# Kernel optimization log

Measured on AMD Instinct MI355X. Metric: run time of the kernel, lower is better.

The kernel has to match this reference:

```python
import jax, jax.numpy as jnp
import numpy as np

jax.config.update("jax_enable_x64", True)  # window_sum runs cumsums in double, as in the torch source

WIN = 7
EPS = 0.01


def _gradient(I):
    # forward finite differences, cropping to [D-1, H-1, W-1] (same=False path, reduction='mean')
    c = I[:, :, 1:, 1:, 1:]
    dx = c - I[:, :, :-1, 1:, 1:]
    dy = c - I[:, :, 1:, :-1, 1:]
    dz = c - I[:, :, 1:, 1:, :-1]
    return dx, dy, dz


def _window_sum(I, win):
    # 3D box-filter via triple cumsum on a zero-padded double-precision volume
    if win == 1:
        return I
    half = win // 2
    pad = (half + win % 2, half)
    Ip = jnp.pad(I, ((0, 0), (0, 0), pad, pad, pad)).astype(jnp.float64)
    cs = jnp.cumsum(jnp.cumsum(jnp.cumsum(Ip, axis=2), axis=3), axis=4)
    x, y, z = I.shape[2:]
    w = win
    out = (cs[:, :, w:, w:, w:] - cs[:, :, w:, w:, :z] - cs[:, :, w:, :y, w:]
           - cs[:, :, :x, w:, w:] + cs[:, :, w:, :y, :z] + cs[:, :, :x, w:, :z]
           + cs[:, :, :x, :y, w:] - cs[:, :, :x, :y, :z])
    return out.astype(jnp.float32)


def setup_inputs() -> dict:
    key = jax.random.key(0)
    k1, k2 = jax.random.split(key)
    shape = (2, 1, 160, 192, 160)
    Ii = jax.random.normal(k1, shape, dtype=jnp.float32)
    Ji = jax.random.normal(k2, shape, dtype=jnp.float32)
    return {"Ii": Ii, "Ji": Ji}


def reference(Ii, Ji):
    def det(dx, dy, dz):
        return dx * dx + dy * dy + dz * dz + EPS

    dxI, dyI, dzI = _gradient(Ii)
    dxJ, dyJ, dzJ = _gradient(Ji)
    dx_I = _window_sum(dxI, WIN)
    dy_I = _window_sum(dyI, WIN)
    dz_I = _window_sum(dzI, WIN)
    dx_J = _window_sum(dxJ, WIN)
    dy_J = _window_sum(dyJ, WIN)
    dz_J = _window_sum(dzJ, WIN)
    cross = jnp.abs(dx_I * dx_J + dy_I * dy_J + dz_I * dz_J) + EPS
    norm = jnp.sqrt(det(dx_I, dy_I, dz_I) * det(dx_J, dy_J, dz_J))
    return jnp.mean(cross / norm)
```

## Files before the change

kernel.cpp:

```cpp
#include <hip/hip_runtime.h>

#define IYD 192
#define IZD 160
#define PLANE 30720
#define VOLSZ 4915200
#define YG 191
#define ZG 159

#define RAWV 660
#define RAWR 44
#define ZBB 1324
#define DBB 2404
#define ZDV 540
#define ZDR 36
#define TBB 3484
#define WBB 3996
#define LDSF 4508

#define NVOX_INV (1.0f / 9657342.0f)

__global__ __launch_bounds__(256, 4) void grad_sim_v7(
    const float* __restrict__ Ii, const float* __restrict__ Ji,
    float* __restrict__ out)
{
    __shared__ __align__(16) float lds[LDSF];
    const int tid = threadIdx.x;
    const int z0 = (int)blockIdx.x * 32;
    const int y0 = (int)blockIdx.y * 8;
    const int seg = blockIdx.z & 3;
    const int bat = blockIdx.z >> 2;
    const int s0 = seg * 40;
    const int a0 = (seg == 0) ? 0 : (s0 - 3);
    const int aLast = (seg == 3) ? 159 : (s0 + 43);

    const float* __restrict__ bI = Ii + (size_t)bat * VOLSZ;
    const float* __restrict__ bJ = Ji + (size_t)bat * VOLSZ;

    const float* gq0;
    const float* gq1;
    int lq0, lq1;
    float mq0, mq1;
    {
        int q = tid;
        int v = q / 150;
        int rr = q - v * 150;
        int row = rr / 10;
        int qd = rr - row * 10;
        int iy = y0 - 3 + row;
        int izb = z0 - 4 + 4 * qd;
        bool ok = ((unsigned)iy < IYD) && (izb >= 0) && (izb + 3 <= 159);
        int iyc = min(max(iy, 0), IYD - 1);
        int izc = min(max(izb, 0), 156);
        gq0 = (v ? bJ : bI) + (iyc * IZD + izc);
        lq0 = v * RAWV + row * RAWR + 4 * qd;
        mq0 = ok ? 1.f : 0.f;
    }
    {
        int q = 256 + tid;
        int v = q / 150;
        int rr = q - v * 150;
        int row = rr / 10;
        int qd = rr - row * 10;
        int iy = y0 - 3 + row;
        int izb = z0 - 4 + 4 * qd;
        bool ok = ((unsigned)iy < IYD) && (izb >= 0) && (izb + 3 <= 159);
        int iyc = min(max(iy, 0), IYD - 1);
        int izc = min(max(izb, 0), 156);
        gq1 = (v ? bJ : bI) + (iyc * IZD + izc);
        lq1 = v * RAWV + row * RAWR + 4 * qd;
        mq1 = ok ? 1.f : 0.f;
    }

    const int zv = tid / 60;
    const int zrr = tid - 60 * zv;
    const int zr = zrr >> 2;
    const int zq = zrr & 3;
    const bool doZ = tid < 120;
    const bool zlo = (z0 == 0) && (zq == 0);
    const bool zhi = (z0 == 128) && (zq == 3);
    const int rawRd = zv * RAWV + zr * RAWR + 8 * zq;
    const int zdWr = zv * ZDV + zr * ZDR + 8 * zq;

    const int e2half = tid & 1;
    const int e2c = tid >> 1;
    const int e2zq = e2c & 7;
    const int e2f = (e2c >> 3) & 1;
    const int e2v = e2c >> 4;
    const bool doY = tid < 64;
    const int e2base = (e2f ? DBB : ZBB) + e2v * ZDV + 4 * e2zq;
    const int e2out = (e2f ? WBB : TBB) + e2v * 256 + 4 * e2zq;
    const float mlo = (y0 == 0) ? 0.f : 1.f;
    const float mhi = (y0 == 184) ? 0.f : 1.f;

    const int oy = tid >> 5;
    const int oz = tid & 31;
    const int ygl = y0 + oy;
    const int vmax = min(3, 190 - ygl);
    const int vmin = max(-3, -ygl);
    const int vHiI = ZBB + (oy + vmax + 4) * ZDR + oz;
    const int vLoI = ZBB + (oy + vmin + 3) * ZDR + oz;
    const bool okyz = (ygl < YG) && ((z0 + oz) < ZG);

    float Tr[2][8], Vr[2][8], Wr[2][8], Sdy[2], Sdz[2];
#pragma unroll
    for (int v = 0; v < 2; ++v) {
#pragma unroll
        for (int j = 0; j < 8; ++j) { Tr[v][j] = 0.f; Vr[v][j] = 0.f; Wr[v][j] = 0.f; }
        Sdy[v] = 0.f; Sdz[v] = 0.f;
    }
    float acc = 0.f;

    {
        const size_t pb = (size_t)a0 * PLANE;
        float4 t0 = *(const float4*)(gq0 + pb);
        t0.x *= mq0; t0.y *= mq0; t0.z *= mq0; t0.w *= mq0;
        *(float4*)&lds[lq0] = t0;
        if (tid < 44) {
            float4 t1 = *(const float4*)(gq1 + pb);
            t1.x *= mq1; t1.y *= mq1; t1.z *= mq1; t1.w *= mq1;
            *(float4*)&lds[lq1] = t1;
        }
    }
    __syncthreads();

    for (int ag = (a0 & ~7); ag <= aLast; ag += 8) {
#pragma unroll
        for (int u = 0; u < 8; ++u) {
            const int a = ag + u;
            if (a < a0 || a > aLast) continue;

            const bool dof = (a + 1) <= aLast;
            float4 pf0, pf1;
            if (dof) {
                const size_t pb = (size_t)(a + 1) * PLANE;
                pf0 = *(const float4*)(gq0 + pb);
                if (tid < 44) pf1 = *(const float4*)(gq1 + pb);
            }

            if (doZ) {
                float C[16];
                const float4* rb = (const float4*)&lds[rawRd];
#pragma unroll
                for (int q = 0; q < 4; ++q) ((float4*)C)[q] = rb[q];
                float D[8];
#pragma unroll
                for (int i = 0; i < 8; ++i) D[i] = C[i + 8] - C[i + 1];
                if (zlo) { D[0] = C[8] - C[4]; D[1] = C[9] - C[4]; D[2] = C[10] - C[4]; }
                if (zhi) { D[4] = C[11] - C[5]; D[5] = C[11] - C[6];
                           D[6] = C[11] - C[7]; D[7] = C[11] - C[8]; }
                if (zlo) { C[2] = 0.f; C[3] = 0.f; C[4] = 0.f; }
                float Z[8];
                float w = C[2] + C[3] + C[4] + C[5] + C[6] + C[7] + C[8];
                Z[0] = w;
#pragma unroll
                for (int m = 1; m < 8; ++m) { w += C[m + 8] - C[m + 1]; Z[m] = w; }
                float4* zb = (float4*)&lds[ZBB + zdWr];
                zb[0] = make_float4(Z[0], Z[1], Z[2], Z[3]);
                zb[1] = make_float4(Z[4], Z[5], Z[6], Z[7]);
                float4* db = (float4*)&lds[DBB + zdWr];
                db[0] = make_float4(D[0], D[1], D[2], D[3]);
                db[1] = make_float4(D[4], D[5], D[6], D[7]);
            }
            __syncthreads();

            if (doY) {
                float4 r[11];
                const int r0 = e2half ? 4 : 1;
#pragma unroll
                for (int i = 0; i < 11; ++i)
                    r[i] = *(const float4*)&lds[e2base + (r0 + i) * ZDR];
                if (e2half == 0) {
                    r[0].x *= mlo; r[0].y *= mlo; r[0].z *= mlo; r[0].w *= mlo;
                    r[1].x *= mlo; r[1].y *= mlo; r[1].z *= mlo; r[1].w *= mlo;
                    r[2].x *= mlo; r[2].y *= mlo; r[2].z *= mlo; r[2].w *= mlo;
                    r[10].x *= mhi; r[10].y *= mhi; r[10].z *= mhi; r[10].w *= mhi;
                    float4 w;
                    w.x = r[0].x + r[1].x + r[2].x + r[3].x + r[4].x + r[5].x + r[6].x;
                    w.y = r[0].y + r[1].y + r[2].y + r[3].y + r[4].y + r[5].y + r[6].y;
                    w.z = r[0].z + r[1].z + r[2].z + r[3].z + r[4].z + r[5].z + r[6].z;
                    w.w = r[0].w + r[1].w + r[2].w + r[3].w + r[4].w + r[5].w + r[6].w;
                    *(float4*)&lds[e2out] = w;
#pragma unroll
                    for (int m = 1; m < 4; ++m) {
                        w.x += r[m + 6].x - r[m - 1].x;
                        w.y += r[m + 6].y - r[m - 1].y;
                        w.z += r[m + 6].z - r[m - 1].z;
                        w.w += r[m + 6].w - r[m - 1].w;
                        *(float4*)&lds[e2out + m * 32] = w;
                    }
                } else {
                    r[7].x *= mhi; r[7].y *= mhi; r[7].z *= mhi; r[7].w *= mhi;
                    r[8].x *= mhi; r[8].y *= mhi; r[8].z *= mhi; r[8].w *= mhi;
                    r[9].x *= mhi; r[9].y *= mhi; r[9].z *= mhi; r[9].w *= mhi;
                    r[10].x *= mhi; r[10].y *= mhi; r[10].z *= mhi; r[10].w *= mhi;
                    float4 w;
                    w.x = r[1].x + r[2].x + r[3].x + r[4].x + r[5].x + r[6].x + r[7].x;
                    w.y = r[1].y + r[2].y + r[3].y + r[4].y + r[5].y + r[6].y + r[7].y;
                    w.z = r[1].z + r[2].z + r[3].z + r[4].z + r[5].z + r[6].z + r[7].z;
                    w.w = r[1].w + r[2].w + r[3].w + r[4].w + r[5].w + r[6].w + r[7].w;
                    *(float4*)&lds[e2out + 4 * 32] = w;
#pragma unroll
                    for (int m = 1; m < 4; ++m) {
                        w.x += r[m + 7].x - r[m].x;
                        w.y += r[m + 7].y - r[m].y;
                        w.z += r[m + 7].z - r[m].z;
                        w.w += r[m + 7].w - r[m].w;
                        *(float4*)&lds[e2out + (4 + m) * 32] = w;
                    }
                }
            }
            __syncthreads();

            {
                float tI = lds[TBB + tid];
                float tJ = lds[TBB + 256 + tid];
                float wI = lds[WBB + tid];
                float wJ = lds[WBB + 256 + tid];
                float vI = lds[vHiI] - lds[vLoI];
                float vJ = lds[vHiI + ZDV] - lds[vLoI + ZDV];
                if (a == a0) { vI = 0.f; vJ = 0.f; wI = 0.f; wJ = 0.f; }
                const int p = u;
                const int p1 = (u + 1) & 7;
                float hdxI = tI - Tr[0][p1];
                float hdxJ = tJ - Tr[1][p1];
                Sdy[0] += vI - Vr[0][p1]; Vr[0][p] = vI;
                Sdy[1] += vJ - Vr[1][p1]; Vr[1][p] = vJ;
                Sdz[0] += wI - Wr[0][p1]; Wr[0][p] = wI;
                Sdz[1] += wJ - Wr[1][p1]; Wr[1][p] = wJ;
                Tr[0][p] = tI; Tr[1][p] = tJ;
                if (p == 0 && a == 0) {
                    Tr[0][5] = tI; Tr[0][6] = tI; Tr[0][7] = tI;
                    Tr[1][5] = tJ; Tr[1][6] = tJ; Tr[1][7] = tJ;
                }
                if (a >= s0 + 4) {
                    float cross = fabsf(hdxI * hdxJ + Sdy[0] * Sdy[1] + Sdz[0] * Sdz[1]) + 0.01f;
                    float dI = hdxI * hdxI + Sdy[0] * Sdy[0] + Sdz[0] * Sdz[0] + 0.01f;
                    float dJ = hdxJ * hdxJ + Sdy[1] * Sdy[1] + Sdz[1] * Sdz[1] + 0.01f;
                    float val = cross * rsqrtf(dI * dJ);
                    if (okyz) acc += val;
                }
            }

            if (dof) {
                pf0.x *= mq0; pf0.y *= mq0; pf0.z *= mq0; pf0.w *= mq0;
                *(float4*)&lds[lq0] = pf0;
                if (tid < 44) {
                    pf1.x *= mq1; pf1.y *= mq1; pf1.z *= mq1; pf1.w *= mq1;
                    *(float4*)&lds[lq1] = pf1;
                }
            }
            __syncthreads();
        }
    }

    if (seg == 3) {
#pragma unroll
        for (int tt = 0; tt < 3; ++tt) {
            const int sl = tt + 1;
            float hdxI = Tr[0][7] - Tr[0][sl];
            float hdxJ = Tr[1][7] - Tr[1][sl];
            Sdy[0] -= Vr[0][sl]; Sdy[1] -= Vr[1][sl];
            Sdz[0] -= Wr[0][sl]; Sdz[1] -= Wr[1][sl];
            float cross = fabsf(hdxI * hdxJ + Sdy[0] * Sdy[1] + Sdz[0] * Sdz[1]) + 0.01f;
            float dI = hdxI * hdxI + Sdy[0] * Sdy[0] + Sdz[0] * Sdz[0] + 0.01f;
            float dJ = hdxJ * hdxJ + Sdy[1] * Sdy[1] + Sdz[1] * Sdz[1] + 0.01f;
            float val = cross * rsqrtf(dI * dJ);
            if (okyz) acc += val;
        }
    }

#pragma unroll
    for (int off = 32; off > 0; off >>= 1) acc += __shfl_down(acc, off, 64);
    __syncthreads();
    if ((tid & 63) == 0) lds[tid >> 6] = acc;
    __syncthreads();
    if (tid == 0)
        atomicAdd(out, (lds[0] + lds[1] + lds[2] + lds[3]) * NVOX_INV);
}

extern "C" void kernel_launch(void* const* d_in, const int* in_sizes, int n_in,
                              void* d_out, int out_size, void* d_ws, size_t ws_size,
                              hipStream_t stream) {
    const float* Ii = (const float*)d_in[0];
    const float* Ji = (const float*)d_in[1];
    float* out = (float*)d_out;
    hipMemsetAsync(d_out, 0, sizeof(float) * (out_size > 0 ? out_size : 1), stream);
    dim3 grid(5, 24, 8);
    grad_sim_v7<<<grid, dim3(256), 0, stream>>>(Ii, Ji, out);
}
```

Baseline: 77.73 us.

## Process two x-planes per barrier phase with double-buffered LDS stages

The plane loop now handles two consecutive x-planes per iteration. It uses double-buffered raw, Z/D and T/W LDS regions, so the z-pass and y-pass for both planes run in parallel across the two halves of the block. This roughly halves the number of __syncthreads per plane and prefetches two planes ahead to deepen the memory pipeline. In exchange, LDS use per block roughly doubles (about 36 KB), which may limit occupancy, and register pressure rises from the extra prefetch registers.

```diff
diff --git a/kernel.cpp b/kernel.cpp
--- a/kernel.cpp
+++ b/kernel.cpp
@@ -9,17 +9,26 @@
 
 #define RAWV 660
 #define RAWR 44
-#define ZBB 1324
-#define DBB 2404
+#define RAWSLOT 1320
+#define ZBA 2668
+#define DBA 3748
+#define ZBB2 4844
+#define DBB2 5924
+#define TBA 7004
+#define WBA 7516
+#define TBB2 8028
+#define WBB2 8540
 #define ZDV 540
 #define ZDR 36
-#define TBB 3484
-#define WBB 3996
-#define LDSF 4508
+#define LDSF 9052
 
 #define NVOX_INV (1.0f / 9657342.0f)
 
-__global__ __launch_bounds__(256, 4) void grad_sim_v7(
+__device__ __forceinline__ float4 f4scale(float4 a, float s) {
+    return make_float4(a.x * s, a.y * s, a.z * s, a.w * s);
+}
+
+__global__ __launch_bounds__(256, 4) void grad_sim_v12(
     const float* __restrict__ Ii, const float* __restrict__ Ji,
     float* __restrict__ out)
 {
@@ -36,59 +45,55 @@
     const float* __restrict__ bI = Ii + (size_t)bat * VOLSZ;
     const float* __restrict__ bJ = Ji + (size_t)bat * VOLSZ;
 
-    const float* gq0;
-    const float* gq1;
-    int lq0, lq1;
-    float mq0, mq1;
+    const float* gq0; const float* gq1;
+    int lq0, lq1; float mq0, mq1;
     {
         int q = tid;
-        int v = q / 150;
-        int rr = q - v * 150;
-        int row = rr / 10;
-        int qd = rr - row * 10;
-        int iy = y0 - 3 + row;
-        int izb = z0 - 4 + 4 * qd;
+        int v = q / 150; int rr = q - v * 150;
+        int row = rr / 10; int qd = rr - row * 10;
+        int iy = y0 - 3 + row; int izb = z0 - 4 + 4 * qd;
         bool ok = ((unsigned)iy < IYD) && (izb >= 0) && (izb + 3 <= 159);
-        int iyc = min(max(iy, 0), IYD - 1);
-        int izc = min(max(izb, 0), 156);
+        int iyc = min(max(iy, 0), IYD - 1); int izc = min(max(izb, 0), 156);
         gq0 = (v ? bJ : bI) + (iyc * IZD + izc);
         lq0 = v * RAWV + row * RAWR + 4 * qd;
         mq0 = ok ? 1.f : 0.f;
     }
     {
         int q = 256 + tid;
-        int v = q / 150;
-        int rr = q - v * 150;
-        int row = rr / 10;
-        int qd = rr - row * 10;
-        int iy = y0 - 3 + row;
-        int izb = z0 - 4 + 4 * qd;
+        int v = q / 150; int rr = q - v * 150;
+        int row = rr / 10; int qd = rr - row * 10;
+        int iy = y0 - 3 + row; int izb = z0 - 4 + 4 * qd;
         bool ok = ((unsigned)iy < IYD) && (izb >= 0) && (izb + 3 <= 159);
-        int iyc = min(max(iy, 0), IYD - 1);
-        int izc = min(max(izb, 0), 156);
+        int iyc = min(max(iy, 0), IYD - 1); int izc = min(max(izb, 0), 156);
         gq1 = (v ? bJ : bI) + (iyc * IZD + izc);
         lq1 = v * RAWV + row * RAWR + 4 * qd;
         mq1 = ok ? 1.f : 0.f;
     }
 
-    const int zv = tid / 60;
-    const int zrr = tid - 60 * zv;
-    const int zr = zrr >> 2;
-    const int zq = zrr & 3;
-    const bool doZ = tid < 120;
+    const int pp = tid >> 7;
+    const int rem = tid & 127;
+    const bool doZ = rem < 120;
+    const int e1t = doZ ? rem : 0;
+    const int zv = (e1t >= 60) ? 1 : 0;
+    const int rr1 = e1t - 60 * zv;
+    const int zr = rr1 >> 2;
+    const int zq = rr1 & 3;
     const bool zlo = (z0 == 0) && (zq == 0);
     const bool zhi = (z0 == 128) && (zq == 3);
-    const int rawRd = zv * RAWV + zr * RAWR + 8 * zq;
-    const int zdWr = zv * ZDV + zr * ZDR + 8 * zq;
-
-    const int e2half = tid & 1;
-    const int e2c = tid >> 1;
+    const int rawRd = pp * RAWSLOT + zv * RAWV + zr * RAWR + 8 * zq;
+    const int zbW = (pp ? ZBB2 : ZBA) + zv * ZDV + zr * ZDR + 8 * zq;
+    const int dbW = (pp ? DBB2 : DBA) + zv * ZDV + zr * ZDR + 8 * zq;
+
+    const int pp2 = (tid >> 6) & 1;
+    const bool doY = tid < 128;
+    const int et = tid & 63;
+    const int e2half = et & 1;
+    const int e2c = et >> 1;
     const int e2zq = e2c & 7;
     const int e2f = (e2c >> 3) & 1;
     const int e2v = e2c >> 4;
-    const bool doY = tid < 64;
-    const int e2base = (e2f ? DBB : ZBB) + e2v * ZDV + 4 * e2zq;
-    const int e2out = (e2f ? WBB : TBB) + e2v * 256 + 4 * e2zq;
+    const int e2base = (e2f ? (pp2 ? DBB2 : DBA) : (pp2 ? ZBB2 : ZBA)) + e2v * ZDV + 4 * e2zq;
+    const int e2out = (e2f ? (pp2 ? WBB2 : WBA) : (pp2 ? TBB2 : TBA)) + e2v * 256 + 4 * e2zq;
     const float mlo = (y0 == 0) ? 0.f : 1.f;
     const float mhi = (y0 == 184) ? 0.f : 1.f;
 
@@ -97,8 +102,8 @@
     const int ygl = y0 + oy;
     const int vmax = min(3, 190 - ygl);
     const int vmin = max(-3, -ygl);
-    const int vHiI = ZBB + (oy + vmax + 4) * ZDR + oz;
-    const int vLoI = ZBB + (oy + vmin + 3) * ZDR + oz;
+    const int vHiRel = (oy + vmax + 4) * ZDR + oz;
+    const int vLoRel = (oy + vmin + 3) * ZDR + oz;
     const bool okyz = (ygl < YG) && ((z0 + oz) < ZG);
 
     float Tr[2][8], Vr[2][8], Wr[2][8], Sdy[2], Sdz[2];
@@ -111,33 +116,47 @@
     float acc = 0.f;
 
     {
-        const size_t pb = (size_t)a0 * PLANE;
-        float4 t0 = *(const float4*)(gq0 + pb);
-        t0.x *= mq0; t0.y *= mq0; t0.z *= mq0; t0.w *= mq0;
-        *(float4*)&lds[lq0] = t0;
-        if (tid < 44) {
-            float4 t1 = *(const float4*)(gq1 + pb);
-            t1.x *= mq1; t1.y *= mq1; t1.z *= mq1; t1.w *= mq1;
-            *(float4*)&lds[lq1] = t1;
+        const size_t pb0 = (size_t)a0 * PLANE;
+        if (a0 & 1) {
+            *(float4*)&lds[RAWSLOT + lq0] = f4scale(*(const float4*)(gq0 + pb0), mq0);
+            if (tid < 44)
+                *(float4*)&lds[RAWSLOT + lq1] = f4scale(*(const float4*)(gq1 + pb0), mq1);
+        } else {
+            *(float4*)&lds[lq0] = f4scale(*(const float4*)(gq0 + pb0), mq0);
+            if (tid < 44)
+                *(float4*)&lds[lq1] = f4scale(*(const float4*)(gq1 + pb0), mq1);
+            const size_t pb1 = (size_t)(a0 + 1) * PLANE;
+            *(float4*)&lds[RAWSLOT + lq0] = f4scale(*(const float4*)(gq0 + pb1), mq0);
+            if (tid < 44)
+                *(float4*)&lds[RAWSLOT + lq1] = f4scale(*(const float4*)(gq1 + pb1), mq1);
         }
     }
     __syncthreads();
 
     for (int ag = (a0 & ~7); ag <= aLast; ag += 8) {
 #pragma unroll
-        for (int u = 0; u < 8; ++u) {
+        for (int uu = 0; uu < 4; ++uu) {
+            const int u = 2 * uu;
             const int a = ag + u;
-            if (a < a0 || a > aLast) continue;
-
-            const bool dof = (a + 1) <= aLast;
-            float4 pf0, pf1;
-            if (dof) {
-                const size_t pb = (size_t)(a + 1) * PLANE;
-                pf0 = *(const float4*)(gq0 + pb);
-                if (tid < 44) pf1 = *(const float4*)(gq1 + pb);
-            }
-
-            if (doZ) {
+            if (a + 1 < a0 || a > aLast) continue;
+            const bool actA = (a >= a0) && (a <= aLast);
+            const bool actB = (a + 1 >= a0) && (a + 1 <= aLast);
+            const bool landA = (a + 2 <= aLast);
+            const bool landB = (a + 3 <= aLast);
+
+            float4 pfA0, pfA1, pfB0, pfB1;
+            if (landA) {
+                const size_t pb = (size_t)(a + 2) * PLANE;
+                pfA0 = *(const float4*)(gq0 + pb);
+                if (tid < 44) pfA1 = *(const float4*)(gq1 + pb);
+            }
+            if (landB) {
+                const size_t pb = (size_t)(a + 3) * PLANE;
+                pfB0 = *(const float4*)(gq0 + pb);
+                if (tid < 44) pfB1 = *(const float4*)(gq1 + pb);
+            }
+
+            if (doZ && (pp ? actB : actA)) {
                 float C[16];
                 const float4* rb = (const float4*)&lds[rawRd];
 #pragma unroll
@@ -154,16 +173,16 @@
                 Z[0] = w;
 #pragma unroll
                 for (int m = 1; m < 8; ++m) { w += C[m + 8] - C[m + 1]; Z[m] = w; }
-                float4* zb = (float4*)&lds[ZBB + zdWr];
+                float4* zb = (float4*)&lds[zbW];
                 zb[0] = make_float4(Z[0], Z[1], Z[2], Z[3]);
                 zb[1] = make_float4(Z[4], Z[5], Z[6], Z[7]);
-                float4* db = (float4*)&lds[DBB + zdWr];
+                float4* db = (float4*)&lds[dbW];
                 db[0] = make_float4(D[0], D[1], D[2], D[3]);
                 db[1] = make_float4(D[4], D[5], D[6], D[7]);
             }
             __syncthreads();
 
-            if (doY) {
+            if (doY && (pp2 ? actB : actA)) {
                 float4 r[11];
                 const int r0 = e2half ? 4 : 1;
 #pragma unroll
@@ -211,13 +230,13 @@
             }
             __syncthreads();
 
-            {
-                float tI = lds[TBB + tid];
-                float tJ = lds[TBB + 256 + tid];
-                float wI = lds[WBB + tid];
-                float wJ = lds[WBB + 256 + tid];
-                float vI = lds[vHiI] - lds[vLoI];
-                float vJ = lds[vHiI + ZDV] - lds[vLoI + ZDV];
+            if (actA) {
+                float tI = lds[TBA + tid];
+                float tJ = lds[TBA + 256 + tid];
+                float wI = lds[WBA + tid];
+                float wJ = lds[WBA + 256 + tid];
+                float vI = lds[ZBA + vHiRel] - lds[ZBA + vLoRel];
+                float vJ = lds[ZBA + ZDV + vHiRel] - lds[ZBA + ZDV + vLoRel];
                 if (a == a0) { vI = 0.f; vJ = 0.f; wI = 0.f; wJ = 0.f; }
                 const int p = u;
                 const int p1 = (u + 1) & 7;
@@ -228,7 +247,7 @@
                 Sdz[0] += wI - Wr[0][p1]; Wr[0][p] = wI;
                 Sdz[1] += wJ - Wr[1][p1]; Wr[1][p] = wJ;
                 Tr[0][p] = tI; Tr[1][p] = tJ;
-                if (p == 0 && a == 0) {
+                if (u == 0 && a == 0) {
                     Tr[0][5] = tI; Tr[0][6] = tI; Tr[0][7] = tI;
                     Tr[1][5] = tJ; Tr[1][6] = tJ; Tr[1][7] = tJ;
                 }
@@ -240,14 +259,39 @@
                     if (okyz) acc += val;
                 }
             }
-
-            if (dof) {
-                pf0.x *= mq0; pf0.y *= mq0; pf0.z *= mq0; pf0.w *= mq0;
-                *(float4*)&lds[lq0] = pf0;
-                if (tid < 44) {
-                    pf1.x *= mq1; pf1.y *= mq1; pf1.z *= mq1; pf1.w *= mq1;
-                    *(float4*)&lds[lq1] = pf1;
+            if (actB) {
+                float tI = lds[TBB2 + tid];
+                float tJ = lds[TBB2 + 256 + tid];
+                float wI = lds[WBB2 + tid];
+                float wJ = lds[WBB2 + 256 + tid];
+                float vI = lds[ZBB2 + vHiRel] - lds[ZBB2 + vLoRel];
+                float vJ = lds[ZBB2 + ZDV + vHiRel] - lds[ZBB2 + ZDV + vLoRel];
+                if (a + 1 == a0) { vI = 0.f; vJ = 0.f; wI = 0.f; wJ = 0.f; }
+                const int p = u + 1;
+                const int p1 = (u + 2) & 7;
+                float hdxI = tI - Tr[0][p1];
+                float hdxJ = tJ - Tr[1][p1];
+                Sdy[0] += vI - Vr[0][p1]; Vr[0][p] = vI;
+                Sdy[1] += vJ - Vr[1][p1]; Vr[1][p] = vJ;
+                Sdz[0] += wI - Wr[0][p1]; Wr[0][p] = wI;
+                Sdz[1] += wJ - Wr[1][p1]; Wr[1][p] = wJ;
+                Tr[0][p] = tI; Tr[1][p] = tJ;
+                if (a + 1 >= s0 + 4) {
+                    float cross = fabsf(hdxI * hdxJ + Sdy[0] * Sdy[1] + Sdz[0] * Sdz[1]) + 0.01f;
+                    float dI = hdxI * hdxI + Sdy[0] * Sdy[0] + Sdz[0] * Sdz[0] + 0.01f;
+                    float dJ = hdxJ * hdxJ + Sdy[1] * Sdy[1] + Sdz[1] * Sdz[1] + 0.01f;
+                    float val = cross * rsqrtf(dI * dJ);
+                    if (okyz) acc += val;
                 }
+            }
+
+            if (landA) {
+                *(float4*)&lds[lq0] = f4scale(pfA0, mq0);
+                if (tid < 44) *(float4*)&lds[lq1] = f4scale(pfA1, mq1);
+            }
+            if (landB) {
+                *(float4*)&lds[RAWSLOT + lq0] = f4scale(pfB0, mq0);
+                if (tid < 44) *(float4*)&lds[RAWSLOT + lq1] = f4scale(pfB1, mq1);
             }
             __syncthreads();
         }
@@ -286,5 +330,5 @@
     float* out = (float*)d_out;
     hipMemsetAsync(d_out, 0, sizeof(float) * (out_size > 0 ? out_size : 1), stream);
     dim3 grid(5, 24, 8);
-    grad_sim_v7<<<grid, dim3(256), 0, stream>>>(Ii, Ji, out);
+    grad_sim_v12<<<grid, dim3(256), 0, stream>>>(Ii, Ji, out);
 }
```

After: 202.6 us. 2.61x slower.
